# Optimization experiments

Hardware: AMD Instinct MI355X
Metric: run time of the kernel (lower is better)

## Reference

```python
import math
import jax, jax.numpy as jnp
import numpy as np

N = 512
C_S, C_Z, C_H, H, PQ, PV = 384, 128, 16, 12, 4, 8
INF, EPS = 1e5, 1e-8


def _quat_to_rot(q):
    # q: [N,4] unnormalized quaternions -> [N,3,3] rotation matrices
    q = q / jnp.linalg.norm(q, axis=-1, keepdims=True)
    w, x, y, z = q[:, 0], q[:, 1], q[:, 2], q[:, 3]
    return jnp.stack([
        jnp.stack([1 - 2 * (y * y + z * z), 2 * (x * y - w * z), 2 * (x * z + w * y)], -1),
        jnp.stack([2 * (x * y + w * z), 1 - 2 * (x * x + z * z), 2 * (y * z - w * x)], -1),
        jnp.stack([2 * (x * z - w * y), 2 * (y * z + w * x), 1 - 2 * (x * x + y * y)], -1),
    ], -2)


def setup_inputs() -> dict:
    key = jax.random.key(0)
    ks = jax.random.split(key, 16)
    sc = 0.02
    inp = {
        "s": jax.random.normal(ks[0], (N, C_S), jnp.float32),
        "z": jax.random.normal(ks[1], (N, N, C_Z), jnp.float32),
        "rot": _quat_to_rot(jax.random.normal(ks[2], (N, 4), jnp.float32)),
        "trans": jax.random.normal(ks[3], (N, 3), jnp.float32) * 10.0,
        "mask": jnp.ones((N,), jnp.float32),
        "Wq": jax.random.normal(ks[4], (C_S, H * C_H), jnp.float32) * sc,
        "bq": jnp.zeros((H * C_H,), jnp.float32),
        "Wkv": jax.random.normal(ks[5], (C_S, 2 * H * C_H), jnp.float32) * sc,
        "bkv": jnp.zeros((2 * H * C_H,), jnp.float32),
        "Wqp": jax.random.normal(ks[6], (C_S, H * 3 * PQ), jnp.float32) * sc,
        "bqp": jnp.zeros((H * 3 * PQ,), jnp.float32),
        "Wkvp": jax.random.normal(ks[7], (C_S, H * 3 * (PQ + PV)), jnp.float32) * sc,
        "bkvp": jnp.zeros((H * 3 * (PQ + PV),), jnp.float32),
        "Wb": jax.random.normal(ks[8], (C_Z, H), jnp.float32) * sc,
        "bb": jnp.zeros((H,), jnp.float32),
        "head_weights": jnp.full((H,), math.log(math.e - 1.0), jnp.float32),
        "Wout": jax.random.normal(ks[9], (H * (C_Z + C_H + PV * 4), C_S), jnp.float32) * sc,
        "bout": jnp.zeros((C_S,), jnp.float32),
    }
    return inp


def _ipa(s, z, rot, trans, mask, Wq, bq, Wkv, bkv, Wqp, bqp, Wkvp, bkvp, Wb, bb, head_weights, Wout, bout):
    q = (s @ Wq + bq).reshape(N, H, C_H)
    kv = (s @ Wkv + bkv).reshape(N, H, 2 * C_H)
    k, v = kv[..., :C_H], kv[..., C_H:]

    def proj_pts(W, b, P):
        # torch: split last dim into 3 chunks, stack on -1 -> layout [N, 3, H, P] -> [N, H, P, 3]
        pl = (s @ W + b).reshape(N, 3, H, P).transpose(0, 2, 3, 1)
        return jnp.einsum('nij,nhpj->nhpi', rot, pl) + trans[:, None, None, :]

    q_pts = proj_pts(Wqp, bqp, PQ)                    # [N,H,PQ,3]
    kv_pts = proj_pts(Wkvp, bkvp, PQ + PV)            # [N,H,PQ+PV,3]
    k_pts, v_pts = kv_pts[..., :PQ, :], kv_pts[..., PQ:, :]

    b_bias = z @ Wb + bb                              # [N,N,H]
    a = jnp.einsum('ihc,jhc->hij', q, k) * math.sqrt(1.0 / (3 * C_H))
    a = a + math.sqrt(1.0 / 3) * b_bias.transpose(2, 0, 1)

    d2 = jnp.sum((q_pts[:, None] - k_pts[None]) ** 2, axis=-1)   # [i,j,H,PQ]
    hw = jax.nn.softplus(head_weights) * math.sqrt(1.0 / (3 * (PQ * 9.0 / 2)))
    pt_att = -0.5 * jnp.sum(d2 * hw[None, None, :, None], axis=-1)  # [i,j,H]

    sq_mask = INF * (mask[:, None] * mask[None, :] - 1.0)
    a = jax.nn.softmax(a + pt_att.transpose(2, 0, 1) + sq_mask[None], axis=-1)  # [H,i,j]

    o = jnp.einsum('hij,jhc->ihc', a, v).reshape(N, H * C_H)
    o_pt = jnp.einsum('hij,jhpc->ihpc', a, v_pts)                 # [i,H,PV,3]
    o_pt = jnp.einsum('nji,nhpj->nhpi', rot, o_pt - trans[:, None, None, :])  # invert_apply
    o_pt_norm = jnp.sqrt(jnp.sum(o_pt ** 2, axis=-1) + EPS).reshape(N, H * PV)
    o_pt_flat = o_pt.reshape(N, H * PV, 3)
    o_pair = jnp.einsum('hij,ijc->ihc', a, z).reshape(N, H * C_Z)

    cat = jnp.concatenate(
        [o, o_pt_flat[..., 0], o_pt_flat[..., 1], o_pt_flat[..., 2], o_pt_norm, o_pair], axis=-1)
    return cat @ Wout + bout


def reference(s, z, rot, trans, mask, Wq, bq, Wkv, bkv, Wqp, bqp, Wkvp, bkvp, Wb, bb, head_weights, Wout, bout):
    return _ipa(s, z, rot, trans, mask, Wq, bq, Wkv, bkv, Wqp, bqp, Wkvp, bkvp, Wb, bb, head_weights, Wout, bout)
```

## Files before the change

### kernel.cpp

```cpp
#include <hip/hip_runtime.h>
#include <math.h>

#define NN 512
#define CS 384
#define CZ 128
#define CH 16
#define HH 12
#define PQ 4
#define PV 8

typedef float f32x4 __attribute__((ext_vector_type(4)));
typedef __bf16 bf16x8 __attribute__((ext_vector_type(8)));

__global__ void k_repack(const float* __restrict__ Wq,  const float* __restrict__ bq,
                         const float* __restrict__ Wkv, const float* __restrict__ bkv,
                         const float* __restrict__ Wqp, const float* __restrict__ bqp,
                         const float* __restrict__ Wkvp,const float* __restrict__ bkvp,
                         float* __restrict__ Wcat, float* __restrict__ bcat)
{
    const int total = CS * 1152;
    for (int idx = blockIdx.x * blockDim.x + threadIdx.x; idx < total; idx += gridDim.x * blockDim.x) {
        int kk = idx / 1152, n = idx % 1152;
        float vv;
        if (n < 192)      vv = Wq  [kk * 192 + n];
        else if (n < 576) vv = Wkv [kk * 384 + (n - 192)];
        else if (n < 720) vv = Wqp [kk * 144 + (n - 576)];
        else              vv = Wkvp[kk * 432 + (n - 720)];
        Wcat[idx] = vv;
    }
    int n = blockIdx.x * blockDim.x + threadIdx.x;
    if (n < 1152) {
        float vv;
        if (n < 192)      vv = bq  [n];
        else if (n < 576) vv = bkv [n - 192];
        else if (n < 720) vv = bqp [n - 576];
        else              vv = bkvp[n - 720];
        bcat[n] = vv;
    }
}

__global__ void k_proj(const float* __restrict__ s, const float* __restrict__ Wcat,
                       const float* __restrict__ bcat,
                       float* __restrict__ q, float* __restrict__ k_t, float* __restrict__ v,
                       float* __restrict__ qp_raw, float* __restrict__ kvp_raw)
{
    __shared__ float As[16 * 68];
    __shared__ float Bs[64 * 64];

    int tx = threadIdx.x & 15;
    int ty = threadIdx.x >> 4;
    int n0 = blockIdx.x * 64;
    int m0 = blockIdx.y * 16;

    float acc[4] = {0.f, 0.f, 0.f, 0.f};

    for (int kb = 0; kb < CS; kb += 64) {
        #pragma unroll
        for (int e = 0; e < 4; ++e) {
            int idx = e * 256 + threadIdx.x;
            int m = idx >> 6, kk = idx & 63;
            As[m * 68 + kk] = s[(size_t)(m0 + m) * CS + kb + kk];
        }
        #pragma unroll
        for (int e = 0; e < 16; ++e) {
            int idx = e * 256 + threadIdx.x;
            int kk = idx >> 6, n = idx & 63;
            Bs[kk * 64 + n] = Wcat[(size_t)(kb + kk) * 1152 + n0 + n];
        }
        __syncthreads();

        for (int kk = 0; kk < 64; kk += 4) {
            f32x4 a = *(const f32x4*)&As[ty * 68 + kk];
            f32x4 b[4];
            #pragma unroll
            for (int kq = 0; kq < 4; ++kq)
                b[kq] = *(const f32x4*)&Bs[(kk + kq) * 64 + tx * 4];
            #pragma unroll
            for (int kq = 0; kq < 4; ++kq)
                #pragma unroll
                for (int cc = 0; cc < 4; ++cc)
                    acc[cc] += a[kq] * b[kq][cc];
        }
        __syncthreads();
    }

    int i = m0 + ty;
    #pragma unroll
    for (int cc = 0; cc < 4; ++cc) {
        int col = n0 + tx * 4 + cc;
        float val = acc[cc] + bcat[col];
        if (col < 192) {
            q[i * 192 + col] = val;
        } else if (col < 576) {
            int lc = col - 192;
            int h = lc / 32, w = lc % 32;
            if (w < CH) k_t[(h * CH + w) * NN + i] = val;
            else        v[(i * HH + h) * CH + (w - CH)] = val;
        } else if (col < 720) {
            qp_raw[i * 144 + (col - 576)] = val;
        } else {
            kvp_raw[i * 432 + (col - 720)] = val;
        }
    }
}

__global__ void k_pts_transform(const float* __restrict__ qp_raw, const float* __restrict__ kvp_raw,
                                const float* __restrict__ rot, const float* __restrict__ trans,
                                float* __restrict__ q_pts, float* __restrict__ k_pts_t,
                                float* __restrict__ v_pts)
{
    int idx = blockIdx.x * blockDim.x + threadIdx.x;
    const int total = NN * HH * 16;
    if (idx >= total) return;
    int i = idx / (HH * 16);
    int r = idx % (HH * 16);
    int h = r / 16;
    int p = r % 16;

    float R[9], t3[3];
    for (int a = 0; a < 9; ++a) R[a] = rot[i * 9 + a];
    for (int a = 0; a < 3; ++a) t3[a] = trans[i * 3 + a];

    float x, y, zc;
    if (p < PQ) {
        x  = qp_raw[i * 144 + 0 * 48 + h * PQ + p];
        y  = qp_raw[i * 144 + 1 * 48 + h * PQ + p];
        zc = qp_raw[i * 144 + 2 * 48 + h * PQ + p];
    } else {
        int pp = p - PQ;
        x  = kvp_raw[i * 432 + 0 * 144 + h * 12 + pp];
        y  = kvp_raw[i * 432 + 1 * 144 + h * 12 + pp];
        zc = kvp_raw[i * 432 + 2 * 144 + h * 12 + pp];
    }
    float ox = R[0] * x + R[1] * y + R[2] * zc + t3[0];
    float oy = R[3] * x + R[4] * y + R[5] * zc + t3[1];
    float oz = R[6] * x + R[7] * y + R[8] * zc + t3[2];

    if (p < PQ) {
        int o = ((i * HH + h) * PQ + p) * 3;
        q_pts[o] = ox; q_pts[o + 1] = oy; q_pts[o + 2] = oz;
    } else {
        int pp = p - PQ;
        if (pp < PQ) {
            int rb = (h * PQ + pp) * 3;
            k_pts_t[(size_t)(rb + 0) * NN + i] = ox;
            k_pts_t[(size_t)(rb + 1) * NN + i] = oy;
            k_pts_t[(size_t)(rb + 2) * NN + i] = oz;
        } else {
            int o = ((i * HH + h) * PV + (pp - PQ)) * 3;
            v_pts[o] = ox; v_pts[o + 1] = oy; v_pts[o + 2] = oz;
        }
    }
}

__global__ void __launch_bounds__(512, 8)
k_attn_part(const float* __restrict__ z, const float* __restrict__ Wb,
            const float* __restrict__ bb,
            const float* __restrict__ q, const float* __restrict__ k_t,
            const float* __restrict__ q_pts, const float* __restrict__ k_pts_t,
            const float* __restrict__ head_weights, const float* __restrict__ mask,
            const float* __restrict__ v, const float* __restrict__ v_pts,
            float* __restrict__ stats, float* __restrict__ part,
            float* __restrict__ opair)
{
    __shared__ float lgs[HH][132];
    __shared__ float q_lds[HH * CH];
    __shared__ float qp_lds[HH * PQ * 3];
    __shared__ float hw_lds[HH];
    __shared__ float bb_l[HH];

    const int i  = blockIdx.x >> 2;
    const int jq = blockIdx.x & 3;
    const int j0 = jq * 128;
    const int tid = threadIdx.x;
    const int lane = tid & 63;
    const int wave = tid >> 6;
    const float* zbase = z + (size_t)i * NN * CZ;

    if (tid < HH * CH)     q_lds[tid]  = q[(size_t)i * HH * CH + tid];
    if (tid < HH * PQ * 3) qp_lds[tid] = q_pts[(size_t)i * HH * PQ * 3 + tid];
    if (tid < HH) {
        float x = head_weights[tid];
        hw_lds[tid] = log1pf(expf(x)) * 0.13608276348795434f;
        bb_l[tid] = bb[tid];
    }
    const float mask_i = mask[i];
    __syncthreads();

    {
        const float b_scale = 0.57735026918962576f;
        const int hcol = lane & 15;
        const int q8 = (lane >> 4) * 8;
        bf16x8 wbf[4];
        #pragma unroll
        for (int kc = 0; kc < 4; ++kc) {
            #pragma unroll
            for (int jj = 0; jj < 8; ++jj) {
                int c = kc * 32 + q8 + jj;
                float wv = (hcol < HH) ? Wb[c * HH + hcol] * b_scale : 0.0f;
                wbf[kc][jj] = (__bf16)wv;
            }
        }
        const int jl0 = wave * 16;
        const float* zrow = zbase + (size_t)(j0 + jl0 + hcol) * CZ;
        f32x4 acc = {0.f, 0.f, 0.f, 0.f};
        #pragma unroll
        for (int kc = 0; kc < 4; ++kc) {
            float4 z0 = *(const float4*)(zrow + kc * 32 + q8);
            float4 z1 = *(const float4*)(zrow + kc * 32 + q8 + 4);
            bf16x8 afrag;
            afrag[0] = (__bf16)z0.x; afrag[1] = (__bf16)z0.y;
            afrag[2] = (__bf16)z0.z; afrag[3] = (__bf16)z0.w;
            afrag[4] = (__bf16)z1.x; afrag[5] = (__bf16)z1.y;
            afrag[6] = (__bf16)z1.z; afrag[7] = (__bf16)z1.w;
            acc = __builtin_amdgcn_mfma_f32_16x16x32_bf16(afrag, wbf[kc], acc, 0, 0, 0);
        }
        if (hcol < HH) {
            #pragma unroll
            for (int r = 0; r < 4; ++r)
                lgs[hcol][jl0 + (lane >> 4) * 4 + r] = acc[r];
        }
    }
    __syncthreads();

    {
        const float qk_scale = 0.14433756729740643f;
        const float b_scale  = 0.57735026918962576f;
        const int cl = tid & 127;
        const int j  = j0 + cl;
        const int hg = tid >> 7;
        const float sqm = 100000.0f * (mask_i * mask[j] - 1.0f);
        #pragma unroll
        for (int hh = 0; hh < 3; ++hh) {
            int h = hg * 3 + hh;
            float accq = 0.f;
            #pragma unroll
            for (int c = 0; c < CH; ++c)
                accq += q_lds[h * CH + c] * k_t[(size_t)(h * CH + c) * NN + j];
            float s2 = 0.f;
            #pragma unroll
            for (int p = 0; p < PQ; ++p) {
                int rb = (h * PQ + p) * 3;
                float dx = qp_lds[rb + 0] - k_pts_t[(size_t)(rb + 0) * NN + j];
                float dy = qp_lds[rb + 1] - k_pts_t[(size_t)(rb + 1) * NN + j];
                float dz = qp_lds[rb + 2] - k_pts_t[(size_t)(rb + 2) * NN + j];
                s2 += dx * dx + dy * dy + dz * dz;
            }
            lgs[h][cl] += accq * qk_scale + b_scale * bb_l[h] - 0.5f * hw_lds[h] * s2 + sqm;
        }
    }
    __syncthreads();

    for (int row = wave; row < HH; row += 8) {
        float v0 = lgs[row][lane];
        float v1 = lgs[row][lane + 64];
        float m = fmaxf(v0, v1);
        #pragma unroll
        for (int off = 32; off >= 1; off >>= 1) m = fmaxf(m, __shfl_xor(m, off));
        float e0 = expf(v0 - m);
        float e1 = expf(v1 - m);
        float ss = e0 + e1;
        #pragma unroll
        for (int off = 32; off >= 1; off >>= 1) ss += __shfl_xor(ss, off);
        lgs[row][lane]      = e0;
        lgs[row][lane + 64] = e1;
        if (lane == 0) {
            size_t sb = ((size_t)(i * 4 + jq) * HH + row) * 2;
            stats[sb]     = m;
            stats[sb + 1] = ss;
        }
    }
    __syncthreads();

    if (tid < 480) {
        float acc = 0.f;
        if (tid < 192) {
            const float* lr = lgs[tid >> 4];
            const float* vp = v + (size_t)j0 * 192 + tid;
            #pragma unroll 4
            for (int j = 0; j < 128; ++j)
                acc += lr[j] * vp[(size_t)j * 192];
        } else {
            int r = tid - 192;
            const float* lr = lgs[r / 24];
            const float* vp = v_pts + (size_t)j0 * 288 + r;
            #pragma unroll 4
            for (int j = 0; j < 128; ++j)
                acc += lr[j] * vp[(size_t)j * 288];
        }
        part[(size_t)(i * 4 + jq) * 480 + tid] = acc;
    }

    {
        int cl = lane & 15;
        int q4 = lane >> 4;
        int ha = (cl < HH) ? cl : (HH - 1);
        int cb = wave * 16 + cl;
        f32x4 pacc = {0.f, 0.f, 0.f, 0.f};
        #pragma unroll
        for (int ks = 0; ks < 4; ++ks) {
            int jb = ks * 32 + q4 * 8;
            f32x4 a0 = *(const f32x4*)&lgs[ha][jb];
            f32x4 a1 = *(const f32x4*)&lgs[ha][jb + 4];
            bf16x8 af;
            af[0] = (__bf16)a0[0]; af[1] = (__bf16)a0[1];
            af[2] = (__bf16)a0[2]; af[3] = (__bf16)a0[3];
            af[4] = (__bf16)a1[0]; af[5] = (__bf16)a1[1];
            af[6] = (__bf16)a1[2]; af[7] = (__bf16)a1[3];
            bf16x8 bf;
            #pragma unroll
            for (int jj = 0; jj < 8; ++jj)
                bf[jj] = (__bf16)zbase[(size_t)(j0 + jb + jj) * CZ + cb];
            pacc = __builtin_amdgcn_mfma_f32_16x16x32_bf16(af, bf, pacc, 0, 0, 0);
        }
        #pragma unroll
        for (int r = 0; r < 4; ++r) {
            int h = q4 * 4 + r;
            if (h < HH)
                opair[(size_t)(i * 4 + jq) * 1536 + h * 128 + cb] = pacc[r];
        }
    }
}

__global__ void __launch_bounds__(512, 8)
k_combine(const float* __restrict__ stats, const float* __restrict__ part,
          const float* __restrict__ opair,
          const float* __restrict__ rot, const float* __restrict__ trans,
          float* __restrict__ cat)
{
    __shared__ float f_lds[HH][4];
    __shared__ float opt_lds[HH * PV * 3];

    const int i = blockIdx.x;
    const int tid = threadIdx.x;

    if (tid < HH) {
        float m[4], s[4];
        #pragma unroll
        for (int qq = 0; qq < 4; ++qq) {
            size_t sb = ((size_t)(i * 4 + qq) * HH + tid) * 2;
            m[qq] = stats[sb];
            s[qq] = stats[sb + 1];
        }
        float M = fmaxf(fmaxf(m[0], m[1]), fmaxf(m[2], m[3]));
        float Z = 0.f;
        float e[4];
        #pragma unroll
        for (int qq = 0; qq < 4; ++qq) { e[qq] = expf(m[qq] - M); Z += s[qq] * e[qq]; }
        float invZ = 1.0f / Z;
        #pragma unroll
        for (int qq = 0; qq < 4; ++qq) f_lds[tid][qq] = e[qq] * invZ;
    }
    __syncthreads();

    if (tid < 480) {
        int h = (tid < 192) ? (tid >> 4) : ((tid - 192) / 24);
        float acc = 0.f;
        #pragma unroll
        for (int qq = 0; qq < 4; ++qq)
            acc += f_lds[h][qq] * part[(size_t)(i * 4 + qq) * 480 + tid];
        if (tid < 192) cat[(size_t)i * 2112 + tid] = acc;
        else           opt_lds[tid - 192] = acc;
    }

    #pragma unroll
    for (int k = 0; k < 3; ++k) {
        int idx = tid + k * 512;
        int h = idx >> 7;
        float acc = 0.f;
        #pragma unroll
        for (int qq = 0; qq < 4; ++qq)
            acc += f_lds[h][qq] * opair[(size_t)(i * 4 + qq) * 1536 + idx];
        cat[(size_t)i * 2112 + 576 + idx] = acc;
    }
    __syncthreads();

    if (tid < HH * PV) {
        int hp = tid;
        float R[9], t3[3];
        #pragma unroll
        for (int a2 = 0; a2 < 9; ++a2) R[a2] = rot[i * 9 + a2];
        #pragma unroll
        for (int a2 = 0; a2 < 3; ++a2) t3[a2] = trans[i * 3 + a2];
        float gx = opt_lds[hp * 3 + 0] - t3[0];
        float gy = opt_lds[hp * 3 + 1] - t3[1];
        float gz = opt_lds[hp * 3 + 2] - t3[2];
        float lx = R[0] * gx + R[3] * gy + R[6] * gz;
        float ly = R[1] * gx + R[4] * gy + R[7] * gz;
        float lz = R[2] * gx + R[5] * gy + R[8] * gz;
        float* crow = cat + (size_t)i * 2112;
        crow[192 + 0 * 96 + hp] = lx;
        crow[192 + 1 * 96 + hp] = ly;
        crow[192 + 2 * 96 + hp] = lz;
        crow[480 + hp] = sqrtf(lx * lx + ly * ly + lz * lz + 1e-8f);
    }
}

__global__ void k_final(const float* __restrict__ cat, const float* __restrict__ Wout,
                        const float* __restrict__ bout, float* __restrict__ out)
{
    __shared__ float As[16 * 52];
    __shared__ float Bs[48 * 64];

    int tx = threadIdx.x & 15;
    int ty = threadIdx.x >> 4;
    int n0 = blockIdx.x * 64;
    int m0 = blockIdx.y * 16;
    int k0 = blockIdx.z * 528;

    float acc[4] = {0.f, 0.f, 0.f, 0.f};

    for (int stage = 0; stage < 11; ++stage) {
        int kb = k0 + stage * 48;
        #pragma unroll
        for (int e = 0; e < 3; ++e) {
            int idx = e * 256 + threadIdx.x;
            int m = idx / 48, kk = idx % 48;
            As[m * 52 + kk] = cat[(size_t)(m0 + m) * 2112 + kb + kk];
        }
        #pragma unroll
        for (int e = 0; e < 12; ++e) {
            int idx = e * 256 + threadIdx.x;
            int kk = idx >> 6, n = idx & 63;
            Bs[kk * 64 + n] = Wout[(size_t)(kb + kk) * 384 + n0 + n];
        }
        __syncthreads();

        for (int kk = 0; kk < 48; kk += 4) {
            f32x4 a = *(const f32x4*)&As[ty * 52 + kk];
            f32x4 b[4];
            #pragma unroll
            for (int kq = 0; kq < 4; ++kq)
                b[kq] = *(const f32x4*)&Bs[(kk + kq) * 64 + tx * 4];
            #pragma unroll
            for (int kq = 0; kq < 4; ++kq)
                #pragma unroll
                for (int cc = 0; cc < 4; ++cc)
                    acc[cc] += a[kq] * b[kq][cc];
        }
        __syncthreads();
    }

    bool add_bias = (blockIdx.z == 0);
    int m = m0 + ty;
    #pragma unroll
    for (int cc = 0; cc < 4; ++cc) {
        int n = n0 + tx * 4 + cc;
        float val = acc[cc] + (add_bias ? bout[n] : 0.f);
        atomicAdd(&out[(size_t)m * 384 + n], val);
    }
}

extern "C" void kernel_launch(void* const* d_in, const int* in_sizes, int n_in,
                              void* d_out, int out_size, void* d_ws, size_t ws_size,
                              hipStream_t stream)
{
    const float* s     = (const float*)d_in[0];
    const float* z     = (const float*)d_in[1];
    const float* rot   = (const float*)d_in[2];
    const float* trans = (const float*)d_in[3];
    const float* mask  = (const float*)d_in[4];
    const float* Wq    = (const float*)d_in[5];
    const float* bq    = (const float*)d_in[6];
    const float* Wkv   = (const float*)d_in[7];
    const float* bkv   = (const float*)d_in[8];
    const float* Wqp   = (const float*)d_in[9];
    const float* bqp   = (const float*)d_in[10];
    const float* Wkvp  = (const float*)d_in[11];
    const float* bkvp  = (const float*)d_in[12];
    const float* Wb    = (const float*)d_in[13];
    const float* bb    = (const float*)d_in[14];
    const float* hw    = (const float*)d_in[15];
    const float* Wout  = (const float*)d_in[16];
    const float* bout  = (const float*)d_in[17];
    float* out = (float*)d_out;

    float* ws = (float*)d_ws;
    float* q       = ws;
    float* k_t     = ws + 98304;
    float* v       = ws + 196608;
    float* qp_raw  = ws + 294912;
    float* kvp_raw = ws + 368640;
    float* q_pts   = ws + 589824;
    float* k_pts_t = ws + 663552;
    float* v_pts   = ws + 737280;
    float* cat     = ws + 884736;
    float* Wcat    = ws + 1966080;
    float* bcat    = ws + 2408448;
    float* stats   = ws + 2409600;
    float* part    = ws + 2458752;
    float* opairb  = ws + 3441792;

    hipMemsetAsync(out, 0, (size_t)NN * CS * sizeof(float), stream);

    hipLaunchKernelGGL(k_repack, dim3(512), dim3(256), 0, stream,
                       Wq, bq, Wkv, bkv, Wqp, bqp, Wkvp, bkvp, Wcat, bcat);
    hipLaunchKernelGGL(k_proj, dim3(18, 32), dim3(256), 0, stream,
                       s, Wcat, bcat, q, k_t, v, qp_raw, kvp_raw);
    hipLaunchKernelGGL(k_pts_transform, dim3(384), dim3(256), 0, stream,
                       qp_raw, kvp_raw, rot, trans, q_pts, k_pts_t, v_pts);
    hipLaunchKernelGGL(k_attn_part, dim3(NN * 4), dim3(512), 0, stream,
                       z, Wb, bb, q, k_t, q_pts, k_pts_t, hw, mask,
                       v, v_pts, stats, part, opairb);
    hipLaunchKernelGGL(k_combine, dim3(NN), dim3(512), 0, stream,
                       stats, part, opairb, rot, trans, cat);
    hipLaunchKernelGGL(k_final, dim3(6, 32, 4), dim3(256), 0, stream, cat, Wout, bout, out);
}
```

Before: 351.9 us.

## Store keys row-major and vectorize logit and value-reduction loads in attention

Keys and key points are now stored per residue (row-major) instead of transposed, so each thread fetches its key row with float4 loads rather than scalar strided loads. The value/point weighted sum is split across four j-subranges per output quad, using float4 loads, with partials kept in shared memory and reduced after an extra barrier. This targets scattered, uncoalesced global loads in the attention-partial kernel. It costs extra shared memory, one more sync, and row-major key reads are strided across lanes, which may hurt coalescing.

```diff
diff --git a/kernel.cpp b/kernel.cpp
--- a/kernel.cpp
+++ b/kernel.cpp
@@ -41,7 +41,7 @@
 
 __global__ void k_proj(const float* __restrict__ s, const float* __restrict__ Wcat,
                        const float* __restrict__ bcat,
-                       float* __restrict__ q, float* __restrict__ k_t, float* __restrict__ v,
+                       float* __restrict__ q, float* __restrict__ k_n, float* __restrict__ v,
                        float* __restrict__ qp_raw, float* __restrict__ kvp_raw)
 {
     __shared__ float As[16 * 68];
@@ -94,7 +94,7 @@
         } else if (col < 576) {
             int lc = col - 192;
             int h = lc / 32, w = lc % 32;
-            if (w < CH) k_t[(h * CH + w) * NN + i] = val;
+            if (w < CH) k_n[(size_t)i * 192 + h * CH + w] = val;
             else        v[(i * HH + h) * CH + (w - CH)] = val;
         } else if (col < 720) {
             qp_raw[i * 144 + (col - 576)] = val;
@@ -106,7 +106,7 @@
 
 __global__ void k_pts_transform(const float* __restrict__ qp_raw, const float* __restrict__ kvp_raw,
                                 const float* __restrict__ rot, const float* __restrict__ trans,
-                                float* __restrict__ q_pts, float* __restrict__ k_pts_t,
+                                float* __restrict__ q_pts, float* __restrict__ k_pts_n,
                                 float* __restrict__ v_pts)
 {
     int idx = blockIdx.x * blockDim.x + threadIdx.x;
@@ -142,10 +142,8 @@
     } else {
         int pp = p - PQ;
         if (pp < PQ) {
-            int rb = (h * PQ + pp) * 3;
-            k_pts_t[(size_t)(rb + 0) * NN + i] = ox;
-            k_pts_t[(size_t)(rb + 1) * NN + i] = oy;
-            k_pts_t[(size_t)(rb + 2) * NN + i] = oz;
+            int o = (size_t)i * 144 + (h * PQ + pp) * 3;
+            k_pts_n[o] = ox; k_pts_n[o + 1] = oy; k_pts_n[o + 2] = oz;
         } else {
             int o = ((i * HH + h) * PV + (pp - PQ)) * 3;
             v_pts[o] = ox; v_pts[o + 1] = oy; v_pts[o + 2] = oz;
@@ -156,8 +154,8 @@
 __global__ void __launch_bounds__(512, 8)
 k_attn_part(const float* __restrict__ z, const float* __restrict__ Wb,
             const float* __restrict__ bb,
-            const float* __restrict__ q, const float* __restrict__ k_t,
-            const float* __restrict__ q_pts, const float* __restrict__ k_pts_t,
+            const float* __restrict__ q, const float* __restrict__ k_n,
+            const float* __restrict__ q_pts, const float* __restrict__ k_pts_n,
             const float* __restrict__ head_weights, const float* __restrict__ mask,
             const float* __restrict__ v, const float* __restrict__ v_pts,
             float* __restrict__ stats, float* __restrict__ part,
@@ -168,6 +166,7 @@
     __shared__ float qp_lds[HH * PQ * 3];
     __shared__ float hw_lds[HH];
     __shared__ float bb_l[HH];
+    __shared__ f32x4 pl[120][4];
 
     const int i  = blockIdx.x >> 2;
     const int jq = blockIdx.x & 3;
@@ -230,22 +229,30 @@
         const int j  = j0 + cl;
         const int hg = tid >> 7;
         const float sqm = 100000.0f * (mask_i * mask[j] - 1.0f);
+        const float* krow = k_n     + (size_t)j * 192 + hg * 48;
+        const float* prow = k_pts_n + (size_t)j * 144 + hg * 36;
         #pragma unroll
         for (int hh = 0; hh < 3; ++hh) {
             int h = hg * 3 + hh;
-            float accq = 0.f;
-            #pragma unroll
-            for (int c = 0; c < CH; ++c)
-                accq += q_lds[h * CH + c] * k_t[(size_t)(h * CH + c) * NN + j];
-            float s2 = 0.f;
-            #pragma unroll
-            for (int p = 0; p < PQ; ++p) {
-                int rb = (h * PQ + p) * 3;
-                float dx = qp_lds[rb + 0] - k_pts_t[(size_t)(rb + 0) * NN + j];
-                float dy = qp_lds[rb + 1] - k_pts_t[(size_t)(rb + 1) * NN + j];
-                float dz = qp_lds[rb + 2] - k_pts_t[(size_t)(rb + 2) * NN + j];
-                s2 += dx * dx + dy * dy + dz * dz;
-            }
+            f32x4 k0 = *(const f32x4*)(krow + hh * 16 + 0);
+            f32x4 k1 = *(const f32x4*)(krow + hh * 16 + 4);
+            f32x4 k2 = *(const f32x4*)(krow + hh * 16 + 8);
+            f32x4 k3 = *(const f32x4*)(krow + hh * 16 + 12);
+            const float* ql = q_lds + h * CH;
+            float accq = ql[0]*k0[0] + ql[1]*k0[1] + ql[2]*k0[2] + ql[3]*k0[3]
+                       + ql[4]*k1[0] + ql[5]*k1[1] + ql[6]*k1[2] + ql[7]*k1[3]
+                       + ql[8]*k2[0] + ql[9]*k2[1] + ql[10]*k2[2] + ql[11]*k2[3]
+                       + ql[12]*k3[0] + ql[13]*k3[1] + ql[14]*k3[2] + ql[15]*k3[3];
+            f32x4 pa = *(const f32x4*)(prow + hh * 12 + 0);
+            f32x4 pb = *(const f32x4*)(prow + hh * 12 + 4);
+            f32x4 pc = *(const f32x4*)(prow + hh * 12 + 8);
+            const float* qh = qp_lds + h * 12;
+            float t0 = qh[0]-pa[0],  t1 = qh[1]-pa[1],  t2 = qh[2]-pa[2],  t3 = qh[3]-pa[3];
+            float t4 = qh[4]-pb[0],  t5 = qh[5]-pb[1],  t6 = qh[6]-pb[2],  t7 = qh[7]-pb[3];
+            float t8 = qh[8]-pc[0],  t9 = qh[9]-pc[1],  t10= qh[10]-pc[2], t11= qh[11]-pc[3];
+            float s2 = t0*t0 + t1*t1 + t2*t2 + t3*t3
+                     + t4*t4 + t5*t5 + t6*t6 + t7*t7
+                     + t8*t8 + t9*t9 + t10*t10 + t11*t11;
             lgs[h][cl] += accq * qk_scale + b_scale * bb_l[h] - 0.5f * hw_lds[h] * s2 + sqm;
         }
     }
@@ -273,22 +280,19 @@
     __syncthreads();
 
     if (tid < 480) {
-        float acc = 0.f;
-        if (tid < 192) {
-            const float* lr = lgs[tid >> 4];
-            const float* vp = v + (size_t)j0 * 192 + tid;
-            #pragma unroll 4
-            for (int j = 0; j < 128; ++j)
-                acc += lr[j] * vp[(size_t)j * 192];
-        } else {
-            int r = tid - 192;
-            const float* lr = lgs[r / 24];
-            const float* vp = v_pts + (size_t)j0 * 288 + r;
-            #pragma unroll 4
-            for (int j = 0; j < 128; ++j)
-                acc += lr[j] * vp[(size_t)j * 288];
-        }
-        part[(size_t)(i * 4 + jq) * 480 + tid] = acc;
+        int f = tid >> 2, jsub = tid & 3;
+        int h = (f < 48) ? (f >> 2) : ((f - 48) / 6);
+        const float* lrj = lgs[h] + jsub * 32;
+        const float* bp;
+        int stride;
+        if (f < 48) { bp = v     + (size_t)j0 * 192 + f * 4;        stride = 192; }
+        else        { bp = v_pts + (size_t)j0 * 288 + (f - 48) * 4; stride = 288; }
+        bp += (size_t)(jsub * 32) * stride;
+        f32x4 acc = {0.f, 0.f, 0.f, 0.f};
+        #pragma unroll 8
+        for (int jj = 0; jj < 32; ++jj)
+            acc += lrj[jj] * *(const f32x4*)(bp + (size_t)jj * stride);
+        pl[f][jsub] = acc;
     }
 
     {
@@ -319,6 +323,12 @@
             if (h < HH)
                 opair[(size_t)(i * 4 + jq) * 1536 + h * 128 + cb] = pacc[r];
         }
+    }
+    __syncthreads();
+
+    if (tid < 120) {
+        f32x4 s = pl[tid][0] + pl[tid][1] + pl[tid][2] + pl[tid][3];
+        *(f32x4*)&part[(size_t)(i * 4 + jq) * 480 + tid * 4] = s;
     }
 }
 
@@ -477,12 +487,12 @@
 
     float* ws = (float*)d_ws;
     float* q       = ws;
-    float* k_t     = ws + 98304;
+    float* k_n     = ws + 98304;
     float* v       = ws + 196608;
     float* qp_raw  = ws + 294912;
     float* kvp_raw = ws + 368640;
     float* q_pts   = ws + 589824;
-    float* k_pts_t = ws + 663552;
+    float* k_pts_n = ws + 663552;
     float* v_pts   = ws + 737280;
     float* cat     = ws + 884736;
     float* Wcat    = ws + 1966080;
@@ -496,11 +506,11 @@
     hipLaunchKernelGGL(k_repack, dim3(512), dim3(256), 0, stream,
                        Wq, bq, Wkv, bkv, Wqp, bqp, Wkvp, bkvp, Wcat, bcat);
     hipLaunchKernelGGL(k_proj, dim3(18, 32), dim3(256), 0, stream,
-                       s, Wcat, bcat, q, k_t, v, qp_raw, kvp_raw);
+                       s, Wcat, bcat, q, k_n, v, qp_raw, kvp_raw);
     hipLaunchKernelGGL(k_pts_transform, dim3(384), dim3(256), 0, stream,
-                       qp_raw, kvp_raw, rot, trans, q_pts, k_pts_t, v_pts);
+                       qp_raw, kvp_raw, rot, trans, q_pts, k_pts_n, v_pts);
     hipLaunchKernelGGL(k_attn_part, dim3(NN * 4), dim3(512), 0, stream,
-                       z, Wb, bb, q, k_t, q_pts, k_pts_t, hw, mask,
+                       z, Wb, bb, q, k_n, q_pts, k_pts_n, hw, mask,
                        v, v_pts, stats, part, opairb);
     hipLaunchKernelGGL(k_combine, dim3(NN), dim3(512), 0, stream,
                        stats, part, opairb, rot, trans, cat);
```

New measurement: 383.4 us. +9.0%, slower.
